# Performance work log

Hardware: AMD Instinct MI355X
Metric: run time of the kernel (lower is better)

## Reference

```python
import jax, jax.numpy as jnp
import numpy as np

B, N, FIN, H, D = 2, 512, 128, 4, 64
NEG_SLOPE = 0.2


def setup_inputs() -> dict:
    key = jax.random.key(0)
    ks = jax.random.split(key, 5)
    x = jax.random.normal(ks[0], (B, N, FIN), dtype=jnp.float32)
    # xavier-ish scaled params
    W_proj = jax.random.normal(ks[1], (H, FIN, D), dtype=jnp.float32) * (1.0 / np.sqrt(FIN + D))
    b_proj = jnp.zeros((H, D), dtype=jnp.float32)
    W_cat_weight = jax.random.normal(ks[2], (H, D, 2 * D), dtype=jnp.float32) * (1.0 / np.sqrt(3 * D))
    W_cat_bias = jnp.zeros((H, D), dtype=jnp.float32)
    a = jax.random.normal(ks[3], (H, D), dtype=jnp.float32) * (1.0 / np.sqrt(D))
    bias_param = jnp.zeros((H * D,), dtype=jnp.float32)
    return {"x": x, "W_proj": W_proj, "b_proj": b_proj,
            "W_cat_weight": W_cat_weight, "W_cat_bias": W_cat_bias,
            "a": a, "bias_param": bias_param}


def reference(x, W_proj, b_proj, W_cat_weight, W_cat_bias, a, bias_param):
    # h[b,h,n,d] = W^h x_n + b^h
    h = jnp.einsum('bni,hid->bhnd', x, W_proj) + b_proj[None, :, None, :]
    d = h.shape[-1]
    # W_cat [h_i || h_j] == W1 h_i + W2 h_j  (avoids O(N^2*2D) concat tensor)
    W1 = W_cat_weight[:, :, :d]   # (H, D, D) acts on source node i
    W2 = W_cat_weight[:, :, d:]   # (H, D, D) acts on target node j
    zi = jnp.einsum('bhnd,hed->bhne', h, W1)  # (B,H,N,D)
    zj = jnp.einsum('bhnd,hed->bhne', h, W2)  # (B,H,N,D)
    # z[b,h,i,j,e] = zi[b,h,i,e] + zj[b,h,j,e] + bias, then LeakyReLU
    z = zi[:, :, :, None, :] + zj[:, :, None, :, :] + W_cat_bias[None, :, None, None, :]
    z = jnp.where(z >= 0, z, NEG_SLOPE * z)
    # e[b,h,i,j] = a_h . z
    e = jnp.einsum('bhije,he->bhij', z, a)
    attn = jax.nn.softmax(e, axis=-1)          # softmax over neighbors j
    out = jnp.einsum('bhij,bhjd->bhid', attn, h)  # (B,H,N,D)
    b_, h_, n_, d_ = out.shape
    out = out.transpose(0, 2, 1, 3).reshape(b_, n_, h_ * d_)  # concat heads
    out = out + bias_param
    return out
```

## Files before the change

kernel.cpp:

```cpp
#include <hip/hip_runtime.h>
#include <hip/hip_bf16.h>

#define NN 512
#define FIN 128
#define HH 4
#define DD 64
#define SW 68


__device__ __forceinline__ float rdlane(float v, int idx) {
    return __int_as_float(__builtin_amdgcn_readlane(__float_as_int(v), idx));
}

__global__ __launch_bounds__(256) void proj_kernel(
    const float* __restrict__ x, const float* __restrict__ Wp,
    const float* __restrict__ bp, const float* __restrict__ Wc,
    const float* __restrict__ Wcb, const float* __restrict__ a,
    float* __restrict__ h_ws, float* __restrict__ azi_ws, float* __restrict__ azj_ws,
    float* __restrict__ adi_ws, float* __restrict__ adj_ws)
{
    int blk = blockIdx.x;
    int bh = blk >> 6;
    int n0 = (blk & 63) << 3;
    int b = bh >> 2, hh = bh & 3;

    __shared__ float xs[8 * FIN];
    __shared__ float hs[8][DD];
    __shared__ float Wcs[DD][2 * DD + 1];

    int t = threadIdx.x;

    ((float4*)xs)[t] = ((const float4*)(x + ((size_t)b * NN + n0) * FIN))[t];
    {
        const float4* wg = (const float4*)(Wc + (size_t)hh * DD * 2 * DD);
        #pragma unroll
        for (int k = 0; k < 8; ++k) {
            int idx = t + 256 * k;
            int r = idx >> 5, c4 = (idx & 31) * 4;
            float4 v = wg[idx];
            Wcs[r][c4] = v.x; Wcs[r][c4 + 1] = v.y;
            Wcs[r][c4 + 2] = v.z; Wcs[r][c4 + 3] = v.w;
        }
    }
    __syncthreads();

    int e = t & 63, w = t >> 6;
    const float* Wph = Wp + (size_t)hh * FIN * DD;
    float bpv = bp[hh * DD + e];
    float acc0 = bpv, acc1 = bpv;
    #pragma unroll 8
    for (int i = 0; i < FIN; ++i) {
        float wv = Wph[i * DD + e];
        acc0 = fmaf(xs[w * FIN + i], wv, acc0);
        acc1 = fmaf(xs[(w + 4) * FIN + i], wv, acc1);
    }
    hs[w][e] = acc0; hs[w + 4][e] = acc1;
    float* hg = h_ws + ((size_t)bh * NN + n0) * DD;
    hg[w * DD + e] = acc0; hg[(w + 4) * DD + e] = acc1;
    __syncthreads();

    float zb = Wcb[hh * DD + e];
    float zi0 = zb, zi1 = zb, zj0 = 0.f, zj1 = 0.f;
    #pragma unroll 8
    for (int d2 = 0; d2 < DD; ++d2) {
        float w1 = Wcs[e][d2];
        float w2 = Wcs[e][DD + d2];
        float h0 = hs[w][d2], h1 = hs[w + 4][d2];
        zi0 = fmaf(h0, w1, zi0); zi1 = fmaf(h1, w1, zi1);
        zj0 = fmaf(h0, w2, zj0); zj1 = fmaf(h1, w2, zj1);
    }

    float av = a[hh * DD + e];
    float p0 = av * zi0, p1 = av * zi1, q0 = av * zj0, q1 = av * zj1;
    #pragma unroll
    for (int off = 32; off; off >>= 1) {
        p0 += __shfl_xor(p0, off); p1 += __shfl_xor(p1, off);
        q0 += __shfl_xor(q0, off); q1 += __shfl_xor(q1, off);
    }
    if (e == 0) {
        adi_ws[bh * NN + n0 + w]     = 0.6f * p0;
        adi_ws[bh * NN + n0 + w + 4] = 0.6f * p1;
        adj_ws[bh * NN + n0 + w]     = 0.6f * q0;
        adj_ws[bh * NN + n0 + w + 4] = 0.6f * q1;
    }

    unsigned long long mask = __ballot(av >= 0.f);
    int np = __popcll(mask);
    int GP = (np + 3) >> 2;
    int below = __popcll(mask & ((1ull << e) - 1ull));
    int slot = (av >= 0.f) ? below : (4 * GP + (e - below));
    float pav = __builtin_fabsf(av);

    float* azib = azi_ws + ((size_t)bh * NN + n0) * SW;
    float* azjb = azj_ws + ((size_t)bh * NN + n0) * SW;
    azib[w * SW + slot]       = pav * zi0;
    azib[(w + 4) * SW + slot] = pav * zi1;
    azjb[w * SW + slot]       = pav * zj0;
    azjb[(w + 4) * SW + slot] = pav * zj1;
    int p1c = 4 * GP - np;
    if (e < 4) {
        int psl = (e < p1c) ? (np + e) : (4 * GP + 64 - np + (e - p1c));
        azib[w * SW + psl] = 0.f; azib[(w + 4) * SW + psl] = 0.f;
        azjb[w * SW + psl] = 0.f; azjb[(w + 4) * SW + psl] = 0.f;
    }
}

#define ZJS 0
#define HS  2176
#define ADJS 4224
#define EPo 4256
__global__ __launch_bounds__(256, 2) void attn9(
    const float* __restrict__ h_ws, const float* __restrict__ azi_ws,
    const float* __restrict__ azj_ws, const float* __restrict__ adi_ws,
    const float* __restrict__ adj_ws, const float* __restrict__ a,
    float* __restrict__ pacc, float* __restrict__ pm, float* __restrict__ ps)
{
    int blk = blockIdx.x;
    int js = blk & 15, is_ = (blk >> 4) & 3, bh = blk >> 6;
    int i0 = is_ << 7, j0 = js << 5, hh = bh & 3;
    int t = threadIdx.x, lane = t & 63;
    int w = __builtin_amdgcn_readfirstlane(t >> 6);

    __shared__ float smem[128 * 72];

    {
        const float4* src = (const float4*)(azi_ws + ((size_t)bh * NN + i0) * SW);
        #pragma unroll
        for (int k = 0; k < 9; ++k) {
            int idx = t + 256 * k;
            if (idx < 2176) {
                int r = idx / 17, c = idx % 17;
                *(float4*)&smem[r * 72 + c * 4] = src[idx];
            }
        }
    }
    __syncthreads();
    float4 ziA[17], ziB[17];
    #pragma unroll
    for (int k = 0; k < 17; ++k) {
        ziA[k] = *(const float4*)&smem[lane * 72 + 4 * k];
        ziB[k] = *(const float4*)&smem[(lane + 64) * 72 + 4 * k];
    }
    float adi0 = adi_ws[bh * NN + i0 + lane];
    float adi1 = adi_ws[bh * NN + i0 + 64 + lane];
    __syncthreads();

    {
        const float4* sj = (const float4*)(azj_ws + ((size_t)bh * NN + j0) * SW);
        #pragma unroll
        for (int k = 0; k < 3; ++k) {
            int idx = t + 256 * k;
            if (idx < 544) ((float4*)&smem[ZJS])[idx] = sj[idx];
        }
        const float4* sh = (const float4*)(h_ws + ((size_t)bh * NN + j0) * DD);
        ((float4*)&smem[HS])[t] = sh[t];
        ((float4*)&smem[HS])[t + 256] = sh[t + 256];
        if (t < 32) smem[ADJS + t] = adj_ws[bh * NN + j0 + t];
    }

    float av_e = a[hh * DD + lane];
    unsigned long long mask = __ballot(av_e >= 0.f);
    int GP = (__popcll(mask) + 3) >> 2;

    __syncthreads();

    #pragma unroll
    for (int jj = 0; jj < 8; ++jj) {
        int j = 8 * w + jj;
        const float4* zjr = (const float4*)&smem[ZJS + j * SW];
        float adjv = smem[ADJS + j];
        float a0 = 0.f, a1 = 0.f, b0 = 0.f, b1 = 0.f;
        #pragma unroll
        for (int k = 0; k < 17; ++k) {
            float4 z = zjr[k];
            float sg = (k < GP) ? 0.4f : -0.4f;
            a0 = fmaf(sg, __builtin_fabsf(ziA[k].x + z.x), a0);
            a1 = fmaf(sg, __builtin_fabsf(ziA[k].y + z.y), a1);
            a0 = fmaf(sg, __builtin_fabsf(ziA[k].z + z.z), a0);
            a1 = fmaf(sg, __builtin_fabsf(ziA[k].w + z.w), a1);
            b0 = fmaf(sg, __builtin_fabsf(ziB[k].x + z.x), b0);
            b1 = fmaf(sg, __builtin_fabsf(ziB[k].y + z.y), b1);
            b0 = fmaf(sg, __builtin_fabsf(ziB[k].z + z.z), b0);
            b1 = fmaf(sg, __builtin_fabsf(ziB[k].w + z.w), b1);
        }
        smem[EPo + j * 132 + lane]      = adi0 + adjv + (a0 + a1);
        smem[EPo + j * 132 + 64 + lane] = adi1 + adjv + (b0 + b1);
    }
    __syncthreads();

    {
        int r = t >> 1, jh = t & 1;
        float e16[16];
        float m = -1e30f;
        #pragma unroll
        for (int jj = 0; jj < 16; ++jj) {
            e16[jj] = smem[EPo + (16 * jh + jj) * 132 + r];
            m = fmaxf(m, e16[jj]);
        }
        m = fmaxf(m, __shfl_xor(m, 1));
        float s = 0.f;
        #pragma unroll
        for (int jj = 0; jj < 16; ++jj) {
            float p = __expf(e16[jj] - m);
            s += p;
            smem[EPo + (16 * jh + jj) * 132 + r] = p;
        }
        s += __shfl_xor(s, 1);
        if (jh == 0) {
            pm[js * 4096 + bh * NN + i0 + r] = m;
            ps[js * 4096 + bh * NN + i0 + r] = s;
        }
    }
    __syncthreads();

    {
        int hi = (w >> 1) * 64;
        int base = (w & 1) * 32;
        float acc[32];
        #pragma unroll
        for (int q = 0; q < 32; ++q) acc[q] = 0.f;
        #pragma unroll 4
        for (int j = 0; j < 32; ++j) {
            float vh = smem[HS + j * 64 + lane];
            float vp = smem[EPo + j * 132 + hi + lane];
            #pragma unroll
            for (int ii = 0; ii < 32; ++ii) {
                float sp = rdlane(vp, base + ii);
                acc[ii] = fmaf(sp, vh, acc[ii]);
            }
        }
        float* pb = pacc + ((size_t)(js * 8 + bh) * NN + i0 + 32 * w) * DD + lane;
        #pragma unroll
        for (int q = 0; q < 32; ++q)
            pb[(size_t)q * DD] = acc[q];
    }
}

__global__ __launch_bounds__(256) void combine_kernel(
    const float* __restrict__ pacc, const float* __restrict__ pm,
    const float* __restrict__ ps, const float* __restrict__ bias_param,
    float* __restrict__ out)
{
    int tid = blockIdx.x * 256 + threadIdx.x;
    int d = tid & 63;
    int row = tid >> 6;
    int bh = row >> 9, n = row & 511;
    int b = bh >> 2, hh = bh & 3;
    float mv[16];
    float m = -1e30f;
    #pragma unroll
    for (int p = 0; p < 16; ++p) { mv[p] = pm[p * 4096 + row]; m = fmaxf(m, mv[p]); }
    float denom = 0.f, acc = 0.f;
    #pragma unroll
    for (int p = 0; p < 16; ++p) {
        float wgt = __expf(mv[p] - m);
        denom = fmaf(ps[p * 4096 + row], wgt, denom);
        acc = fmaf(pacc[(size_t)p * 262144 + (size_t)row * 64 + d], wgt, acc);
    }
    out[((size_t)b * NN + n) * (HH * DD) + hh * DD + d] =
        acc / denom + bias_param[hh * DD + d];
}

extern "C" void kernel_launch(void* const* d_in, const int* in_sizes, int n_in,
                              void* d_out, int out_size, void* d_ws, size_t ws_size,
                              hipStream_t stream) {
    const float* x    = (const float*)d_in[0];
    const float* Wp   = (const float*)d_in[1];
    const float* bp   = (const float*)d_in[2];
    const float* Wc   = (const float*)d_in[3];
    const float* Wcb  = (const float*)d_in[4];
    const float* a    = (const float*)d_in[5];
    const float* bpar = (const float*)d_in[6];
    float* out = (float*)d_out;

    float* ws     = (float*)d_ws;
    float* h_ws   = ws;
    float* azi_ws = ws + 262144;
    float* azj_ws = ws + 540672;
    float* adi_ws = ws + 819200;
    float* adj_ws = ws + 823296;
    float* pacc   = ws + 827392;
    float* pm     = ws + 5021696;
    float* ps     = ws + 5087232;

    proj_kernel<<<dim3(512), dim3(256), 0, stream>>>(
        x, Wp, bp, Wc, Wcb, a, h_ws, azi_ws, azj_ws, adi_ws, adj_ws);
    attn9<<<dim3(512), dim3(256), 0, stream>>>(
        h_ws, azi_ws, azj_ws, adi_ws, adj_ws, a, pacc, pm, ps);
    combine_kernel<<<dim3(1024), dim3(256), 0, stream>>>(
        pacc, pm, ps, bpar, out);
}
```

Before: 48.75 us.

## Use chunk-major azi/azj layout and 512-thread attention blocks reading zi from LDS

The projection kernel now writes the absolute-scaled zi/zj vectors in a chunk-major layout (17 float4 chunks by node) instead of padded rows. The attention kernel moves to 512 threads with each wave handling 4 j columns, and it streams zi from LDS per chunk rather than holding 34 float4 registers per thread. This cuts register pressure so more waves can be resident, and gives coalesced global and LDS loads. Softmax and the P·V stage are re-split to four threads per row and 16 rows per wave. In exchange LDS use per block grows, which may limit how many blocks fit per CU.

```diff
diff --git a/kernel.cpp b/kernel.cpp
--- a/kernel.cpp
+++ b/kernel.cpp
@@ -16,7 +16,7 @@
     const float* __restrict__ x, const float* __restrict__ Wp,
     const float* __restrict__ bp, const float* __restrict__ Wc,
     const float* __restrict__ Wcb, const float* __restrict__ a,
-    float* __restrict__ h_ws, float* __restrict__ azi_ws, float* __restrict__ azj_ws,
+    float* __restrict__ h_ws, float* __restrict__ azi_c, float* __restrict__ azj_c,
     float* __restrict__ adi_ws, float* __restrict__ adj_ws)
 {
     int blk = blockIdx.x;
@@ -91,122 +91,126 @@
     int slot = (av >= 0.f) ? below : (4 * GP + (e - below));
     float pav = __builtin_fabsf(av);
 
-    float* azib = azi_ws + ((size_t)bh * NN + n0) * SW;
-    float* azjb = azj_ws + ((size_t)bh * NN + n0) * SW;
-    azib[w * SW + slot]       = pav * zi0;
-    azib[(w + 4) * SW + slot] = pav * zi1;
-    azjb[w * SW + slot]       = pav * zj0;
-    azjb[(w + 4) * SW + slot] = pav * zj1;
+    {
+        size_t a0 = ((size_t)(bh * 17 + (slot >> 2)) * NN + n0 + w) * 4 + (slot & 3);
+        size_t a1 = ((size_t)(bh * 17 + (slot >> 2)) * NN + n0 + w + 4) * 4 + (slot & 3);
+        azi_c[a0] = pav * zi0; azi_c[a1] = pav * zi1;
+        azj_c[a0] = pav * zj0; azj_c[a1] = pav * zj1;
+    }
     int p1c = 4 * GP - np;
     if (e < 4) {
         int psl = (e < p1c) ? (np + e) : (4 * GP + 64 - np + (e - p1c));
-        azib[w * SW + psl] = 0.f; azib[(w + 4) * SW + psl] = 0.f;
-        azjb[w * SW + psl] = 0.f; azjb[(w + 4) * SW + psl] = 0.f;
-    }
-}
-
-#define ZJS 0
-#define HS  2176
-#define ADJS 4224
-#define EPo 4256
-__global__ __launch_bounds__(256, 2) void attn9(
-    const float* __restrict__ h_ws, const float* __restrict__ azi_ws,
-    const float* __restrict__ azj_ws, const float* __restrict__ adi_ws,
+        size_t a0 = ((size_t)(bh * 17 + (psl >> 2)) * NN + n0 + w) * 4 + (psl & 3);
+        size_t a1 = ((size_t)(bh * 17 + (psl >> 2)) * NN + n0 + w + 4) * 4 + (psl & 3);
+        azi_c[a0] = 0.f; azi_c[a1] = 0.f;
+        azj_c[a0] = 0.f; azj_c[a1] = 0.f;
+    }
+}
+
+#define AZIC 0
+#define ZJC  8704
+#define HSo  10880
+#define ADJo 12928
+#define EPo  12960
+__global__ __launch_bounds__(512, 4) void attn10(
+    const float* __restrict__ h_ws, const float* __restrict__ azi_c,
+    const float* __restrict__ azj_c, const float* __restrict__ adi_ws,
     const float* __restrict__ adj_ws, const float* __restrict__ a,
     float* __restrict__ pacc, float* __restrict__ pm, float* __restrict__ ps)
 {
     int blk = blockIdx.x;
     int js = blk & 15, is_ = (blk >> 4) & 3, bh = blk >> 6;
     int i0 = is_ << 7, j0 = js << 5, hh = bh & 3;
-    int t = threadIdx.x, lane = t & 63;
-    int w = __builtin_amdgcn_readfirstlane(t >> 6);
-
-    __shared__ float smem[128 * 72];
-
-    {
-        const float4* src = (const float4*)(azi_ws + ((size_t)bh * NN + i0) * SW);
-        #pragma unroll
-        for (int k = 0; k < 9; ++k) {
-            int idx = t + 256 * k;
+    int t = threadIdx.x, lane = t & 63, w = t >> 6;
+
+    __shared__ float smem[17184];
+
+    {
+        float4* dstA = (float4*)(smem + AZIC);
+        #pragma unroll
+        for (int k = 0; k < 5; ++k) {
+            int idx = t + 512 * k;
             if (idx < 2176) {
-                int r = idx / 17, c = idx % 17;
-                *(float4*)&smem[r * 72 + c * 4] = src[idx];
+                int c = idx >> 7, r = idx & 127;
+                dstA[idx] = ((const float4*)azi_c)[(size_t)(bh * 17 + c) * NN + i0 + r];
             }
         }
-    }
-    __syncthreads();
-    float4 ziA[17], ziB[17];
-    #pragma unroll
-    for (int k = 0; k < 17; ++k) {
-        ziA[k] = *(const float4*)&smem[lane * 72 + 4 * k];
-        ziB[k] = *(const float4*)&smem[(lane + 64) * 72 + 4 * k];
-    }
-    float adi0 = adi_ws[bh * NN + i0 + lane];
-    float adi1 = adi_ws[bh * NN + i0 + 64 + lane];
-    __syncthreads();
-
-    {
-        const float4* sj = (const float4*)(azj_ws + ((size_t)bh * NN + j0) * SW);
-        #pragma unroll
-        for (int k = 0; k < 3; ++k) {
-            int idx = t + 256 * k;
-            if (idx < 544) ((float4*)&smem[ZJS])[idx] = sj[idx];
-        }
-        const float4* sh = (const float4*)(h_ws + ((size_t)bh * NN + j0) * DD);
-        ((float4*)&smem[HS])[t] = sh[t];
-        ((float4*)&smem[HS])[t + 256] = sh[t + 256];
-        if (t < 32) smem[ADJS + t] = adj_ws[bh * NN + j0 + t];
+        float4* dstJ = (float4*)(smem + ZJC);
+        #pragma unroll
+        for (int k = 0; k < 2; ++k) {
+            int idx = t + 512 * k;
+            if (idx < 544) {
+                int c = idx >> 5, r = idx & 31;
+                dstJ[idx] = ((const float4*)azj_c)[(size_t)(bh * 17 + c) * NN + j0 + r];
+            }
+        }
+        ((float4*)(smem + HSo))[t] =
+            ((const float4*)(h_ws + ((size_t)bh * NN + j0) * DD))[t];
+        if (t < 32) smem[ADJo + t] = adj_ws[bh * NN + j0 + t];
     }
 
     float av_e = a[hh * DD + lane];
     unsigned long long mask = __ballot(av_e >= 0.f);
     int GP = (__popcll(mask) + 3) >> 2;
 
-    __syncthreads();
-
-    #pragma unroll
-    for (int jj = 0; jj < 8; ++jj) {
-        int j = 8 * w + jj;
-        const float4* zjr = (const float4*)&smem[ZJS + j * SW];
-        float adjv = smem[ADJS + j];
-        float a0 = 0.f, a1 = 0.f, b0 = 0.f, b1 = 0.f;
-        #pragma unroll
-        for (int k = 0; k < 17; ++k) {
-            float4 z = zjr[k];
-            float sg = (k < GP) ? 0.4f : -0.4f;
-            a0 = fmaf(sg, __builtin_fabsf(ziA[k].x + z.x), a0);
-            a1 = fmaf(sg, __builtin_fabsf(ziA[k].y + z.y), a1);
-            a0 = fmaf(sg, __builtin_fabsf(ziA[k].z + z.z), a0);
-            a1 = fmaf(sg, __builtin_fabsf(ziA[k].w + z.w), a1);
-            b0 = fmaf(sg, __builtin_fabsf(ziB[k].x + z.x), b0);
-            b1 = fmaf(sg, __builtin_fabsf(ziB[k].y + z.y), b1);
-            b0 = fmaf(sg, __builtin_fabsf(ziB[k].z + z.z), b0);
-            b1 = fmaf(sg, __builtin_fabsf(ziB[k].w + z.w), b1);
-        }
-        smem[EPo + j * 132 + lane]      = adi0 + adjv + (a0 + a1);
-        smem[EPo + j * 132 + 64 + lane] = adi1 + adjv + (b0 + b1);
-    }
-    __syncthreads();
-
-    {
-        int r = t >> 1, jh = t & 1;
-        float e16[16];
+    float adi0 = adi_ws[bh * NN + i0 + lane];
+    float adi1 = adi_ws[bh * NN + i0 + 64 + lane];
+
+    __syncthreads();
+
+    {
+        float accA[4] = {0.f, 0.f, 0.f, 0.f};
+        float accB[4] = {0.f, 0.f, 0.f, 0.f};
+        const float4* AZ = (const float4*)(smem + AZIC);
+        const float4* ZJ = (const float4*)(smem + ZJC);
+        #pragma unroll
+        for (int c = 0; c < 17; ++c) {
+            float4 zA = AZ[c * 128 + lane];
+            float4 zB = AZ[c * 128 + 64 + lane];
+            float sg = (c < GP) ? 0.4f : -0.4f;
+            #pragma unroll
+            for (int j4 = 0; j4 < 4; ++j4) {
+                float4 zj = ZJ[c * 32 + 4 * w + j4];
+                accA[j4] = fmaf(sg, __builtin_fabsf(zA.x + zj.x), accA[j4]);
+                accA[j4] = fmaf(sg, __builtin_fabsf(zA.y + zj.y), accA[j4]);
+                accA[j4] = fmaf(sg, __builtin_fabsf(zA.z + zj.z), accA[j4]);
+                accA[j4] = fmaf(sg, __builtin_fabsf(zA.w + zj.w), accA[j4]);
+                accB[j4] = fmaf(sg, __builtin_fabsf(zB.x + zj.x), accB[j4]);
+                accB[j4] = fmaf(sg, __builtin_fabsf(zB.y + zj.y), accB[j4]);
+                accB[j4] = fmaf(sg, __builtin_fabsf(zB.z + zj.z), accB[j4]);
+                accB[j4] = fmaf(sg, __builtin_fabsf(zB.w + zj.w), accB[j4]);
+            }
+        }
+        #pragma unroll
+        for (int j4 = 0; j4 < 4; ++j4) {
+            float adjv = smem[ADJo + 4 * w + j4];
+            smem[EPo + (4 * w + j4) * 132 + lane]      = adi0 + adjv + accA[j4];
+            smem[EPo + (4 * w + j4) * 132 + 64 + lane] = adi1 + adjv + accB[j4];
+        }
+    }
+    __syncthreads();
+
+    {
+        int r = t >> 2, jq = t & 3;
+        float e8[8];
         float m = -1e30f;
         #pragma unroll
-        for (int jj = 0; jj < 16; ++jj) {
-            e16[jj] = smem[EPo + (16 * jh + jj) * 132 + r];
-            m = fmaxf(m, e16[jj]);
+        for (int jj = 0; jj < 8; ++jj) {
+            e8[jj] = smem[EPo + (8 * jq + jj) * 132 + r];
+            m = fmaxf(m, e8[jj]);
         }
         m = fmaxf(m, __shfl_xor(m, 1));
+        m = fmaxf(m, __shfl_xor(m, 2));
         float s = 0.f;
         #pragma unroll
-        for (int jj = 0; jj < 16; ++jj) {
-            float p = __expf(e16[jj] - m);
+        for (int jj = 0; jj < 8; ++jj) {
+            float p = __expf(e8[jj] - m);
             s += p;
-            smem[EPo + (16 * jh + jj) * 132 + r] = p;
+            smem[EPo + (8 * jq + jj) * 132 + r] = p;
         }
         s += __shfl_xor(s, 1);
-        if (jh == 0) {
+        s += __shfl_xor(s, 2);
+        if (jq == 0) {
             pm[js * 4096 + bh * NN + i0 + r] = m;
             ps[js * 4096 + bh * NN + i0 + r] = s;
         }
@@ -214,25 +218,21 @@
     __syncthreads();
 
     {
-        int hi = (w >> 1) * 64;
-        int base = (w & 1) * 32;
-        float acc[32];
-        #pragma unroll
-        for (int q = 0; q < 32; ++q) acc[q] = 0.f;
+        float acc[16];
+        #pragma unroll
+        for (int ii = 0; ii < 16; ++ii) acc[ii] = 0.f;
         #pragma unroll 4
         for (int j = 0; j < 32; ++j) {
-            float vh = smem[HS + j * 64 + lane];
-            float vp = smem[EPo + j * 132 + hi + lane];
+            float vh = smem[HSo + j * 64 + lane];
+            float vp = smem[EPo + j * 132 + 16 * w + (lane & 15)];
             #pragma unroll
-            for (int ii = 0; ii < 32; ++ii) {
-                float sp = rdlane(vp, base + ii);
-                acc[ii] = fmaf(sp, vh, acc[ii]);
-            }
-        }
-        float* pb = pacc + ((size_t)(js * 8 + bh) * NN + i0 + 32 * w) * DD + lane;
-        #pragma unroll
-        for (int q = 0; q < 32; ++q)
-            pb[(size_t)q * DD] = acc[q];
+            for (int ii = 0; ii < 16; ++ii)
+                acc[ii] = fmaf(rdlane(vp, ii), vh, acc[ii]);
+        }
+        float* pb = pacc + ((size_t)(js * 8 + bh) * NN + i0 + 16 * w) * DD + lane;
+        #pragma unroll
+        for (int ii = 0; ii < 16; ++ii)
+            pb[(size_t)ii * DD] = acc[ii];
     }
 }
 
@@ -275,8 +275,8 @@
 
     float* ws     = (float*)d_ws;
     float* h_ws   = ws;
-    float* azi_ws = ws + 262144;
-    float* azj_ws = ws + 540672;
+    float* azi_c  = ws + 262144;
+    float* azj_c  = ws + 540672;
     float* adi_ws = ws + 819200;
     float* adj_ws = ws + 823296;
     float* pacc   = ws + 827392;
@@ -284,9 +284,9 @@
     float* ps     = ws + 5087232;
 
     proj_kernel<<<dim3(512), dim3(256), 0, stream>>>(
-        x, Wp, bp, Wc, Wcb, a, h_ws, azi_ws, azj_ws, adi_ws, adj_ws);
-    attn9<<<dim3(512), dim3(256), 0, stream>>>(
-        h_ws, azi_ws, azj_ws, adi_ws, adj_ws, a, pacc, pm, ps);
+        x, Wp, bp, Wc, Wcb, a, h_ws, azi_c, azj_c, adi_ws, adj_ws);
+    attn10<<<dim3(512), dim3(512), 0, stream>>>(
+        h_ws, azi_c, azj_c, adi_ws, adj_ws, a, pacc, pm, ps);
     combine_kernel<<<dim3(1024), dim3(256), 0, stream>>>(
         pacc, pm, ps, bpar, out);
 }
```

After: 44.87 us. 8.0% less time.
